# Kernel optimization log

Hardware: AMD Instinct MI355X
Metric: run time of the kernel (lower is better)

Reference implementation:

```python
import jax, jax.numpy as jnp
import numpy as np

B, N, C, K, OUT = 8, 16384, 64, 16, 64
BN_EPS = 1e-5


def setup_inputs() -> dict:
    key = jax.random.key(0)
    k1, k2, k3 = jax.random.split(key, 3)
    x = jax.random.normal(k1, (B, N, C), dtype=jnp.float32)
    idx = jax.random.randint(k2, (B, N, K), 0, N, dtype=jnp.int64)
    # fc weight, stored as (in, out) so y = agg @ W (torch Linear is x @ W.T)
    W = jax.random.normal(k3, (C, OUT), dtype=jnp.float32) * (1.0 / np.sqrt(C))
    gamma = jnp.ones((OUT,), dtype=jnp.float32)
    beta = jnp.zeros((OUT,), dtype=jnp.float32)
    return {"x": x, "idx": idx, "W": W, "gamma": gamma, "beta": beta}


def reference(x, idx, W, gamma, beta):
    Bq, Nq, Cq = x.shape
    Kq = idx.shape[-1]
    # gather neighbor features: (B, N*K, C)
    nbr = jnp.take_along_axis(x, idx.reshape(Bq, Nq * Kq, 1), axis=1)
    nbr = nbr.reshape(Bq, Nq, Kq, Cq)
    # max over neighbors, then relu
    agg = jax.nn.relu(jnp.max(nbr, axis=2))  # (B, N, C)
    # linear (no bias)
    y = agg.reshape(Bq * Nq, Cq) @ W  # (B*N, OUT)
    # BatchNorm1d in training mode: batch stats over rows, biased variance
    mean = jnp.mean(y, axis=0)
    var = jnp.mean((y - mean) ** 2, axis=0)
    y = (y - mean) * jax.lax.rsqrt(var + BN_EPS) * gamma + beta
    return y.reshape(Bq, Nq, -1)
```

## Files before the change

kernel.cpp:

```cpp
#include <hip/hip_runtime.h>

namespace {
constexpr int NPTS = 16384;
constexpr int CH   = 64;
constexpr int KNN  = 16;
constexpr int ROWS = 8 * NPTS;
constexpr float EPS = 1e-5f;
constexpr int NBLK = 1024;
constexpr int NBUCK = 16;
}

typedef __attribute__((ext_vector_type(8))) short  short8;
typedef __attribute__((ext_vector_type(4))) float  f32x4;
typedef __attribute__((ext_vector_type(4))) unsigned uint4v;
typedef __attribute__((ext_vector_type(2))) unsigned uint2v;
typedef __attribute__((ext_vector_type(4))) int    int4v;

static __device__ __forceinline__ unsigned pk_bf16(float lo, float hi) {
    unsigned r;
    asm("v_cvt_pk_bf16_f32 %0, %1, %2" : "=v"(r) : "v"(lo), "v"(hi));
    return r;
}

#define PKM(D, A, B) asm volatile("v_pk_max_i16 %0, %1, %2" : "=v"(D) : "v"(A), "v"(B))

static __device__ __host__ __forceinline__ unsigned f2bf(float f) {
    unsigned u = __builtin_bit_cast(unsigned, f);
    return (u + 0x7fffu + ((u >> 16) & 1u)) >> 16;
}

static __device__ __forceinline__ void prep_wfrags(const float* __restrict__ W,
                                                   unsigned* __restrict__ wsb, int l)
{
    const int nq = l >> 4, nr = l & 15;
#pragma unroll
    for (int ct = 0; ct < 4; ++ct)
#pragma unroll
        for (int kh = 0; kh < 2; ++kh) {
            uint4v d;
#pragma unroll
            for (int dj = 0; dj < 4; ++dj) {
                const int k0 = kh * 32 + nq * 8 + dj * 2;
                unsigned lo = f2bf(W[(size_t)k0 * CH + ct * 16 + nr]);
                unsigned hi = f2bf(W[(size_t)(k0 + 1) * CH + ct * 16 + nr]);
                d[dj] = lo | (hi << 16);
            }
            ((uint4v*)wsb)[(ct * 2 + kh) * 64 + l] = d;
        }
}

__global__ __launch_bounds__(256)
void k_cvt(const float* __restrict__ x, unsigned* __restrict__ xb16,
           const float* __restrict__ W, unsigned* __restrict__ wsb,
           float* __restrict__ stats16)
{
    if (blockIdx.x == 0) {
        if (threadIdx.x < 64) prep_wfrags(W, wsb, threadIdx.x);
        for (int i = threadIdx.x; i < NBUCK * 128; i += 256) stats16[i] = 0.f;
    }
    const int batch = blockIdx.x & 7;
    const int chunk = blockIdx.x >> 3;
    const int lane8 = threadIdx.x & 7;
    const int rr    = threadIdx.x >> 3;
    const float*  xb = x    + (size_t)batch * NPTS * CH;
    unsigned*     ob = xb16 + (size_t)batch * NPTS * 32;
#pragma unroll
    for (int h = 0; h < 2; ++h) {
        const int row = chunk * 64 + h * 32 + rr;
        const f32x4* src = (const f32x4*)(xb + (size_t)row * CH + lane8 * 8);
        f32x4 v0 = src[0], v1 = src[1];
        uint4v d;
        d[0] = pk_bf16(v0[0], v0[1]);
        d[1] = pk_bf16(v0[2], v0[3]);
        d[2] = pk_bf16(v1[0], v1[1]);
        d[3] = pk_bf16(v1[2], v1[3]);
        *(uint4v*)(ob + (size_t)row * 32 + lane8 * 4) = d;
    }
}

__global__ __launch_bounds__(256)
void k_fused_bf16(const unsigned* __restrict__ xb16, const int* __restrict__ idx,
                  const unsigned* __restrict__ wsb, unsigned* __restrict__ yp,
                  float* __restrict__ stats16)
{
    __shared__ __align__(16) ushort   Atile[4][16 * 64];
    __shared__ __align__(16) int      Ibuf[4][256];
    __shared__ __align__(16) unsigned Blds[2048];
    __shared__ float bs1[64], bs2[64];

    const int lane  = threadIdx.x & 63;
    const int wave  = threadIdx.x >> 6;
    const int batch = blockIdx.x & 7;
    const int chunk = blockIdx.x >> 3;

    ((uint4v*)Blds)[threadIdx.x]       = ((const uint4v*)wsb)[threadIdx.x];
    ((uint4v*)Blds)[threadIdx.x + 256] = ((const uint4v*)wsb)[threadIdx.x + 256];
    if (threadIdx.x < 64)       bs1[threadIdx.x] = 0.f;
    else if (threadIdx.x < 128) bs2[threadIdx.x - 64] = 0.f;
    __syncthreads();

    const unsigned* __restrict__ xb = xb16 + (size_t)batch * NPTS * 32;
    const int*      __restrict__ ib = idx  + (size_t)batch * NPTS * KNN;
    unsigned*       __restrict__ yb = yp   + (size_t)batch * NPTS * 32;

    const int r0 = chunk * 128 + wave * 16;
    const int g8 = lane >> 3, c8 = lane & 7;
    const int c4 = lane & 15, qq = lane >> 4;
    const unsigned off16 = (unsigned)c8 * 16u;
    const int key = (c4 & 7) << 4;
    char* aw = (char*)&Atile[wave][0];

    short8 bfr[8];
#pragma unroll
    for (int f = 0; f < 8; ++f)
        bfr[f] = __builtin_bit_cast(short8, ((const uint4v*)Blds)[f * 64 + lane]);

    float sC1[4] = {0.f, 0.f, 0.f, 0.f};
    float sC2[4] = {0.f, 0.f, 0.f, 0.f};

    int4v iq0 = ((const int4v*)(ib + (size_t)r0 * KNN))[lane];
    *(int4v*)&Ibuf[wave][lane * 4] = iq0;
    const int4v* Ip = (const int4v*)&Ibuf[wave][0];
    int ia[16], ibx[16];
    *(int4v*)&ia[0]  = Ip[g8 * 4 + 0];       *(int4v*)&ia[4]  = Ip[g8 * 4 + 1];
    *(int4v*)&ia[8]  = Ip[g8 * 4 + 2];       *(int4v*)&ia[12] = Ip[g8 * 4 + 3];
    *(int4v*)&ibx[0] = Ip[(g8 + 8) * 4 + 0]; *(int4v*)&ibx[4] = Ip[(g8 + 8) * 4 + 1];
    *(int4v*)&ibx[8] = Ip[(g8 + 8) * 4 + 2]; *(int4v*)&ibx[12]= Ip[(g8 + 8) * 4 + 3];

    uint4v va[16], vb[16];
#pragma unroll
    for (int j = 0; j < 16; ++j)
        asm volatile("global_load_dwordx4 %0, %1, %2"
                     : "=v"(va[j]) : "v"((unsigned)ia[j] * 128u + off16), "s"(xb));
#pragma unroll
    for (int j = 0; j < 16; ++j)
        asm volatile("global_load_dwordx4 %0, %1, %2"
                     : "=v"(vb[j]) : "v"((unsigned)ibx[j] * 128u + off16), "s"(xb));

    int4v iq1 = ((const int4v*)(ib + (size_t)(r0 + 64) * KNN))[lane];

    asm volatile("s_waitcnt vmcnt(0)" ::: "memory");
    __builtin_amdgcn_sched_barrier(0);

    uint4v accA = {0, 0, 0, 0}, accB = {0, 0, 0, 0};
#pragma unroll
    for (int j = 0; j < 16; ++j) {
        PKM(accA[0], accA[0], va[j][0]); PKM(accA[1], accA[1], va[j][1]);
        PKM(accA[2], accA[2], va[j][2]); PKM(accA[3], accA[3], va[j][3]);
    }
#pragma unroll
    for (int j = 0; j < 16; ++j) {
        PKM(accB[0], accB[0], vb[j][0]); PKM(accB[1], accB[1], vb[j][1]);
        PKM(accB[2], accB[2], vb[j][2]); PKM(accB[3], accB[3], vb[j][3]);
    }

    *(int4v*)&Ibuf[wave][lane * 4] = iq1;
    *(int4v*)&ia[0]  = Ip[g8 * 4 + 0];       *(int4v*)&ia[4]  = Ip[g8 * 4 + 1];
    *(int4v*)&ia[8]  = Ip[g8 * 4 + 2];       *(int4v*)&ia[12] = Ip[g8 * 4 + 3];
    *(int4v*)&ibx[0] = Ip[(g8 + 8) * 4 + 0]; *(int4v*)&ibx[4] = Ip[(g8 + 8) * 4 + 1];
    *(int4v*)&ibx[8] = Ip[(g8 + 8) * 4 + 2]; *(int4v*)&ibx[12]= Ip[(g8 + 8) * 4 + 3];

#pragma unroll
    for (int j = 0; j < 16; ++j)
        asm volatile("global_load_dwordx4 %0, %1, %2"
                     : "=v"(va[j]) : "v"((unsigned)ia[j] * 128u + off16), "s"(xb));
#pragma unroll
    for (int j = 0; j < 16; ++j)
        asm volatile("global_load_dwordx4 %0, %1, %2"
                     : "=v"(vb[j]) : "v"((unsigned)ibx[j] * 128u + off16), "s"(xb));
    __builtin_amdgcn_sched_barrier(0);

#define TILE_TAIL(RBASE)                                                            \
    {                                                                               \
        *(uint4v*)(aw + ((g8 * 128 + c8 * 16) ^ (g8 << 4)))       = accA;           \
        *(uint4v*)(aw + (((g8 + 8) * 128 + c8 * 16) ^ (g8 << 4))) = accB;           \
        short8 a0 = *(const short8*)(aw + ((c4 * 128 + qq * 16) ^ key));            \
        short8 a1 = *(const short8*)(aw + ((c4 * 128 + 64 + qq * 16) ^ key));       \
        f32x4 acc0 = {0,0,0,0}, acc1 = {0,0,0,0}, acc2 = {0,0,0,0}, acc3 = {0,0,0,0}; \
        acc0 = __builtin_amdgcn_mfma_f32_16x16x32_bf16(a0, bfr[0], acc0, 0, 0, 0);  \
        acc0 = __builtin_amdgcn_mfma_f32_16x16x32_bf16(a1, bfr[1], acc0, 0, 0, 0);  \
        acc1 = __builtin_amdgcn_mfma_f32_16x16x32_bf16(a0, bfr[2], acc1, 0, 0, 0);  \
        acc1 = __builtin_amdgcn_mfma_f32_16x16x32_bf16(a1, bfr[3], acc1, 0, 0, 0);  \
        acc2 = __builtin_amdgcn_mfma_f32_16x16x32_bf16(a0, bfr[4], acc2, 0, 0, 0);  \
        acc2 = __builtin_amdgcn_mfma_f32_16x16x32_bf16(a1, bfr[5], acc2, 0, 0, 0);  \
        acc3 = __builtin_amdgcn_mfma_f32_16x16x32_bf16(a0, bfr[6], acc3, 0, 0, 0);  \
        acc3 = __builtin_amdgcn_mfma_f32_16x16x32_bf16(a1, bfr[7], acc3, 0, 0, 0);  \
        unsigned* ypr = yb + (size_t)((RBASE) + qq * 4) * 32 + c4 * 2;              \
        { uint2v pr; pr[0] = pk_bf16(acc0[0], acc1[0]);                             \
          pr[1] = pk_bf16(acc2[0], acc3[0]); *(uint2v*)(ypr + 0)  = pr; }           \
        { uint2v pr; pr[0] = pk_bf16(acc0[1], acc1[1]);                             \
          pr[1] = pk_bf16(acc2[1], acc3[1]); *(uint2v*)(ypr + 32) = pr; }           \
        { uint2v pr; pr[0] = pk_bf16(acc0[2], acc1[2]);                             \
          pr[1] = pk_bf16(acc2[2], acc3[2]); *(uint2v*)(ypr + 64) = pr; }           \
        { uint2v pr; pr[0] = pk_bf16(acc0[3], acc1[3]);                             \
          pr[1] = pk_bf16(acc2[3], acc3[3]); *(uint2v*)(ypr + 96) = pr; }           \
        sC1[0] += (acc0[0] + acc0[1]) + (acc0[2] + acc0[3]);                        \
        sC2[0] += (acc0[0]*acc0[0] + acc0[1]*acc0[1]) + (acc0[2]*acc0[2] + acc0[3]*acc0[3]); \
        sC1[1] += (acc1[0] + acc1[1]) + (acc1[2] + acc1[3]);                        \
        sC2[1] += (acc1[0]*acc1[0] + acc1[1]*acc1[1]) + (acc1[2]*acc1[2] + acc1[3]*acc1[3]); \
        sC1[2] += (acc2[0] + acc2[1]) + (acc2[2] + acc2[3]);                        \
        sC2[2] += (acc2[0]*acc2[0] + acc2[1]*acc2[1]) + (acc2[2]*acc2[2] + acc2[3]*acc2[3]); \
        sC1[3] += (acc3[0] + acc3[1]) + (acc3[2] + acc3[3]);                        \
        sC2[3] += (acc3[0]*acc3[0] + acc3[1]*acc3[1]) + (acc3[2]*acc3[2] + acc3[3]*acc3[3]); \
    }

    TILE_TAIL(r0)

    asm volatile("s_waitcnt vmcnt(4)" ::: "memory");
    __builtin_amdgcn_sched_barrier(0);

    accA[0] = accA[1] = accA[2] = accA[3] = 0u;
    accB[0] = accB[1] = accB[2] = accB[3] = 0u;
#pragma unroll
    for (int j = 0; j < 16; ++j) {
        PKM(accA[0], accA[0], va[j][0]); PKM(accA[1], accA[1], va[j][1]);
        PKM(accA[2], accA[2], va[j][2]); PKM(accA[3], accA[3], va[j][3]);
    }
#pragma unroll
    for (int j = 0; j < 16; ++j) {
        PKM(accB[0], accB[0], vb[j][0]); PKM(accB[1], accB[1], vb[j][1]);
        PKM(accB[2], accB[2], vb[j][2]); PKM(accB[3], accB[3], vb[j][3]);
    }

    TILE_TAIL(r0 + 64)
#undef TILE_TAIL

#pragma unroll
    for (int ct = 0; ct < 4; ++ct) {
        float s1 = sC1[ct], s2 = sC2[ct];
        s1 += __shfl_xor(s1, 16); s1 += __shfl_xor(s1, 32);
        s2 += __shfl_xor(s2, 16); s2 += __shfl_xor(s2, 32);
        if (lane < 16) {
            atomicAdd(&bs1[ct * 16 + lane], s1);
            atomicAdd(&bs2[ct * 16 + lane], s2);
        }
    }
    __syncthreads();
    if (threadIdx.x < 128)
        atomicAdd(&stats16[(blockIdx.x & (NBUCK - 1)) * 128 + threadIdx.x],
                  (threadIdx.x < 64) ? bs1[threadIdx.x] : bs2[threadIdx.x - 64]);
}

__global__ __launch_bounds__(256)
void k_norm_bf16(const unsigned* __restrict__ yp, float* __restrict__ y,
                 const float* __restrict__ stats16,
                 const float* __restrict__ gamma, const float* __restrict__ beta)
{
    __shared__ float s[CH], b[CH];
    if (threadIdx.x < CH) {
        const int l = threadIdx.x;
        float s1 = 0.f, s2 = 0.f;
#pragma unroll
        for (int k = 0; k < NBUCK; ++k) {
            s1 += stats16[k * 128 + l];
            s2 += stats16[k * 128 + 64 + l];
        }
        const float inv_n = 1.0f / (float)ROWS;
        float mean = s1 * inv_n;
        float var  = s2 * inv_n - mean * mean;
        float sc   = gamma[l] * rsqrtf(var + EPS);
        s[l] = sc;
        b[l] = beta[l] - mean * sc;
    }
    __syncthreads();

    const size_t ntot = (size_t)ROWS * 16;
    size_t i = (size_t)blockIdx.x * blockDim.x + threadIdx.x;
    const size_t stride = (size_t)gridDim.x * blockDim.x;
    for (; i < ntot; i += stride) {
        const size_t row = i >> 4;
        const int c4 = (int)i & 15;
        uint2v p = *(const uint2v*)(yp + row * 32 + c4 * 2);
        float v0 = __uint_as_float(p[0] << 16);
        float v1 = __uint_as_float(p[0] & 0xffff0000u);
        float v2 = __uint_as_float(p[1] << 16);
        float v3 = __uint_as_float(p[1] & 0xffff0000u);
        float* yr = y + row * CH;
        yr[c4]      = fmaf(v0, s[c4],      b[c4]);
        yr[c4 + 16] = fmaf(v1, s[c4 + 16], b[c4 + 16]);
        yr[c4 + 32] = fmaf(v2, s[c4 + 32], b[c4 + 32]);
        yr[c4 + 48] = fmaf(v3, s[c4 + 48], b[c4 + 48]);
    }
}

__global__ __launch_bounds__(64)
void k_prep_fb(const float* __restrict__ W, unsigned* __restrict__ wsb,
               float* __restrict__ stats)
{
    if (threadIdx.x < 64) {
        stats[threadIdx.x] = 0.f;
        stats[64 + threadIdx.x] = 0.f;
        prep_wfrags(W, wsb, threadIdx.x);
    }
}

__global__ __launch_bounds__(256)
void k_fused_f32(const float* __restrict__ x, const int* __restrict__ idx,
                 const unsigned* __restrict__ wsb, float* __restrict__ y,
                 float* __restrict__ stats)
{
    __shared__ __align__(16) ushort Atile[4][16 * 64];
    __shared__ __align__(16) int    Ibuf[4][256];
    __shared__ float bs1[64], bs2[64];

    const int lane  = threadIdx.x & 63;
    const int wave  = threadIdx.x >> 6;
    const int batch = blockIdx.x & 7;
    const int chunk = blockIdx.x >> 3;

    if (threadIdx.x < 64)       bs1[threadIdx.x] = 0.f;
    else if (threadIdx.x < 128) bs2[threadIdx.x - 64] = 0.f;
    __syncthreads();

    const int r0 = chunk * 64 + wave * 16;
    const float* __restrict__ xb = x   + (size_t)batch * NPTS * CH;
    const int*   __restrict__ ib = idx + (size_t)batch * NPTS * KNN;
    float*       __restrict__ yb = y   + (size_t)batch * NPTS * CH;

    const int c4 = lane & 15;
    const int qq = lane >> 4;

    int4v iq = ((const int4v*)(ib + (size_t)r0 * KNN))[lane];
    *(int4v*)&Ibuf[wave][lane * 4] = iq;

    short8 bfr[8];
#pragma unroll
    for (int f = 0; f < 8; ++f)
        bfr[f] = __builtin_bit_cast(short8, ((const uint4v*)wsb)[f * 64 + lane]);

    char* aw = (char*)&Atile[wave][0];
    const f32x4* xb4 = (const f32x4*)xb;

#pragma unroll
    for (int g = 0; g < 4; ++g) {
        const int row = 4 * g + qq;
        const int* ip = &Ibuf[wave][row * KNN];
        f32x4 acc = {0.f, 0.f, 0.f, 0.f};
#pragma unroll
        for (int j = 0; j < KNN; ++j) {
            const int n = ip[j];
            f32x4 v = xb4[n * 16 + c4];
            acc[0] = fmaxf(acc[0], v[0]);
            acc[1] = fmaxf(acc[1], v[1]);
            acc[2] = fmaxf(acc[2], v[2]);
            acc[3] = fmaxf(acc[3], v[3]);
        }
        uint2v pw;
        pw[0] = pk_bf16(acc[0], acc[1]);
        pw[1] = pk_bf16(acc[2], acc[3]);
        const int wb = ((row * 128) + c4 * 8) ^ ((row & 7) << 4);
        *(uint2v*)(aw + wb) = pw;
    }

    const int key = (c4 & 7) << 4;
    short8 a0 = *(const short8*)(aw + ((c4 * 128 + qq * 16) ^ key));
    short8 a1 = *(const short8*)(aw + ((c4 * 128 + 64 + qq * 16) ^ key));

    f32x4 acc0 = {0,0,0,0}, acc1 = {0,0,0,0}, acc2 = {0,0,0,0}, acc3 = {0,0,0,0};
    acc0 = __builtin_amdgcn_mfma_f32_16x16x32_bf16(a0, bfr[0], acc0, 0, 0, 0);
    acc0 = __builtin_amdgcn_mfma_f32_16x16x32_bf16(a1, bfr[1], acc0, 0, 0, 0);
    acc1 = __builtin_amdgcn_mfma_f32_16x16x32_bf16(a0, bfr[2], acc1, 0, 0, 0);
    acc1 = __builtin_amdgcn_mfma_f32_16x16x32_bf16(a1, bfr[3], acc1, 0, 0, 0);
    acc2 = __builtin_amdgcn_mfma_f32_16x16x32_bf16(a0, bfr[4], acc2, 0, 0, 0);
    acc2 = __builtin_amdgcn_mfma_f32_16x16x32_bf16(a1, bfr[5], acc2, 0, 0, 0);
    acc3 = __builtin_amdgcn_mfma_f32_16x16x32_bf16(a0, bfr[6], acc3, 0, 0, 0);
    acc3 = __builtin_amdgcn_mfma_f32_16x16x32_bf16(a1, bfr[7], acc3, 0, 0, 0);

    float* yrow = yb + (size_t)(r0 + qq * 4) * CH + c4;
#define DO_CT(CT, ACC)                                                              \
    {                                                                               \
        yrow[0 * CH + CT * 16] = ACC[0];                                            \
        yrow[1 * CH + CT * 16] = ACC[1];                                            \
        yrow[2 * CH + CT * 16] = ACC[2];                                            \
        yrow[3 * CH + CT * 16] = ACC[3];                                            \
        float s1 = (ACC[0] + ACC[1]) + (ACC[2] + ACC[3]);                           \
        float s2 = (ACC[0]*ACC[0] + ACC[1]*ACC[1]) + (ACC[2]*ACC[2] + ACC[3]*ACC[3]); \
        s1 += __shfl_xor(s1, 16); s1 += __shfl_xor(s1, 32);                         \
        s2 += __shfl_xor(s2, 16); s2 += __shfl_xor(s2, 32);                         \
        if (lane < 16) {                                                            \
            atomicAdd(&bs1[CT * 16 + lane], s1);                                    \
            atomicAdd(&bs2[CT * 16 + lane], s2);                                    \
        }                                                                           \
    }
    DO_CT(0, acc0) DO_CT(1, acc1) DO_CT(2, acc2) DO_CT(3, acc3)
#undef DO_CT

    __syncthreads();
    if (threadIdx.x < 64)        atomicAdd(&stats[threadIdx.x], bs1[threadIdx.x]);
    else if (threadIdx.x < 128)  atomicAdd(&stats[threadIdx.x], bs2[threadIdx.x - 64]);
}

__global__ __launch_bounds__(256)
void k_norm_f32(float* __restrict__ y, const float* __restrict__ stats,
                const float* __restrict__ gamma, const float* __restrict__ beta)
{
    __shared__ float s[CH], b[CH];
    if (threadIdx.x < CH) {
        const int l = threadIdx.x;
        const float inv_n = 1.0f / (float)ROWS;
        float mean = stats[l] * inv_n;
        float var  = stats[64 + l] * inv_n - mean * mean;
        float sc   = gamma[l] * rsqrtf(var + EPS);
        s[l] = sc;
        b[l] = beta[l] - mean * sc;
    }
    __syncthreads();

    f32x4* p = (f32x4*)y;
    const size_t ntot = (size_t)ROWS * CH / 4;
    size_t i = (size_t)blockIdx.x * blockDim.x + threadIdx.x;
    const size_t stride = (size_t)gridDim.x * blockDim.x;
    for (; i < ntot; i += stride) {
        f32x4 v = p[i];
        const int c0 = ((int)i & 15) * 4;
        v[0] = fmaf(v[0], s[c0],     b[c0]);
        v[1] = fmaf(v[1], s[c0 + 1], b[c0 + 1]);
        v[2] = fmaf(v[2], s[c0 + 2], b[c0 + 2]);
        v[3] = fmaf(v[3], s[c0 + 3], b[c0 + 3]);
        p[i] = v;
    }
}

extern "C" void kernel_launch(void* const* d_in, const int* in_sizes, int n_in,
                              void* d_out, int out_size, void* d_ws, size_t ws_size,
                              hipStream_t stream)
{
    const float* x     = (const float*)d_in[0];
    const int*   idx   = (const int*)d_in[1];
    const float* W     = (const float*)d_in[2];
    const float* gamma = (const float*)d_in[3];
    const float* beta  = (const float*)d_in[4];

    float*    y       = (float*)d_out;
    float*    stats   = (float*)d_ws;
    unsigned* wsb     = (unsigned*)(stats + 256);
    char*     base    = (char*)d_ws + 16384;
    unsigned* xb16    = (unsigned*)base;
    float*    stats16 = (float*)(base + (size_t)ROWS * CH * 2);
    unsigned* yp      = (unsigned*)(stats16 + NBUCK * 128);

    const size_t need = 16384 + (size_t)ROWS * CH * 2
                      + (size_t)NBUCK * 128 * 4 + (size_t)ROWS * CH * 2;

    if (ws_size >= need) {
        k_cvt<<<dim3(2048), dim3(256), 0, stream>>>(x, xb16, W, wsb, stats16);
        k_fused_bf16<<<dim3(NBLK), dim3(256), 0, stream>>>(xb16, idx, wsb, yp, stats16);
        k_norm_bf16<<<dim3(2048), dim3(256), 0, stream>>>(yp, y, stats16, gamma, beta);
    } else {
        k_prep_fb<<<dim3(1), dim3(64), 0, stream>>>(W, wsb, stats);
        k_fused_f32<<<dim3(2048), dim3(256), 0, stream>>>(x, idx, wsb, y, stats);
        k_norm_f32<<<dim3(2048), dim3(256), 0, stream>>>(y, stats, gamma, beta);
    }
}
```

Baseline: 41.22 us.

## Process four row-tiles per block with deeper software-pipelined gather loads

Halves the block count and has each wave handle four 64-row tiles instead of two. The gather loads for the next tile, and the index load for the tile after it, are issued before the current tile's MFMA and store tail runs, using fine-grained vmcnt waits. The aim is to hide gather latency and amortise per-block setup: the weight-fragment LDS load and the stats atomics. The cost is fewer blocks in flight, which may reduce occupancy-based latency hiding, and a vmcnt accounting that must match the store counts exactly.

```diff
diff --git a/kernel.cpp b/kernel.cpp
--- a/kernel.cpp
+++ b/kernel.cpp
@@ -6,7 +6,7 @@
 constexpr int KNN  = 16;
 constexpr int ROWS = 8 * NPTS;
 constexpr float EPS = 1e-5f;
-constexpr int NBLK = 1024;
+constexpr int NBLK = 512;
 constexpr int NBUCK = 16;
 }
 
@@ -27,6 +27,29 @@
 static __device__ __host__ __forceinline__ unsigned f2bf(float f) {
     unsigned u = __builtin_bit_cast(unsigned, f);
     return (u + 0x7fffu + ((u >> 16) & 1u)) >> 16;
+}
+
+#define DRAIN(N)                                                  \
+    asm volatile("s_waitcnt vmcnt(" #N ")" ::: "memory");         \
+    __builtin_amdgcn_sched_barrier(0)
+
+static __device__ __forceinline__ void issue16(uint4v* v, const int* ix,
+                                               unsigned off16,
+                                               const unsigned* __restrict__ xb)
+{
+#pragma unroll
+    for (int j = 0; j < 16; ++j)
+        asm volatile("global_load_dwordx4 %0, %1, %2"
+                     : "=v"(v[j]) : "v"((unsigned)ix[j] * 128u + off16), "s"(xb));
+}
+
+static __device__ __forceinline__ void red16(uint4v& acc, const uint4v* v)
+{
+#pragma unroll
+    for (int j = 0; j < 16; ++j) {
+        PKM(acc[0], acc[0], v[j][0]); PKM(acc[1], acc[1], v[j][1]);
+        PKM(acc[2], acc[2], v[j][2]); PKM(acc[3], acc[3], v[j][3]);
+    }
 }
 
 static __device__ __forceinline__ void prep_wfrags(const float* __restrict__ W,
@@ -103,7 +126,7 @@
     const int*      __restrict__ ib = idx  + (size_t)batch * NPTS * KNN;
     unsigned*       __restrict__ yb = yp   + (size_t)batch * NPTS * 32;
 
-    const int r0 = chunk * 128 + wave * 16;
+    const int r0 = chunk * 256 + wave * 16;
     const int g8 = lane >> 3, c8 = lane & 7;
     const int c4 = lane & 15, qq = lane >> 4;
     const unsigned off16 = (unsigned)c8 * 16u;
@@ -118,57 +141,24 @@
     float sC1[4] = {0.f, 0.f, 0.f, 0.f};
     float sC2[4] = {0.f, 0.f, 0.f, 0.f};
 
-    int4v iq0 = ((const int4v*)(ib + (size_t)r0 * KNN))[lane];
-    *(int4v*)&Ibuf[wave][lane * 4] = iq0;
     const int4v* Ip = (const int4v*)&Ibuf[wave][0];
     int ia[16], ibx[16];
-    *(int4v*)&ia[0]  = Ip[g8 * 4 + 0];       *(int4v*)&ia[4]  = Ip[g8 * 4 + 1];
-    *(int4v*)&ia[8]  = Ip[g8 * 4 + 2];       *(int4v*)&ia[12] = Ip[g8 * 4 + 3];
-    *(int4v*)&ibx[0] = Ip[(g8 + 8) * 4 + 0]; *(int4v*)&ibx[4] = Ip[(g8 + 8) * 4 + 1];
-    *(int4v*)&ibx[8] = Ip[(g8 + 8) * 4 + 2]; *(int4v*)&ibx[12]= Ip[(g8 + 8) * 4 + 3];
-
     uint4v va[16], vb[16];
-#pragma unroll
-    for (int j = 0; j < 16; ++j)
-        asm volatile("global_load_dwordx4 %0, %1, %2"
-                     : "=v"(va[j]) : "v"((unsigned)ia[j] * 128u + off16), "s"(xb));
-#pragma unroll
-    for (int j = 0; j < 16; ++j)
-        asm volatile("global_load_dwordx4 %0, %1, %2"
-                     : "=v"(vb[j]) : "v"((unsigned)ibx[j] * 128u + off16), "s"(xb));
-
-    int4v iq1 = ((const int4v*)(ib + (size_t)(r0 + 64) * KNN))[lane];
-
-    asm volatile("s_waitcnt vmcnt(0)" ::: "memory");
-    __builtin_amdgcn_sched_barrier(0);
-
-    uint4v accA = {0, 0, 0, 0}, accB = {0, 0, 0, 0};
-#pragma unroll
-    for (int j = 0; j < 16; ++j) {
-        PKM(accA[0], accA[0], va[j][0]); PKM(accA[1], accA[1], va[j][1]);
-        PKM(accA[2], accA[2], va[j][2]); PKM(accA[3], accA[3], va[j][3]);
-    }
-#pragma unroll
-    for (int j = 0; j < 16; ++j) {
-        PKM(accB[0], accB[0], vb[j][0]); PKM(accB[1], accB[1], vb[j][1]);
-        PKM(accB[2], accB[2], vb[j][2]); PKM(accB[3], accB[3], vb[j][3]);
-    }
-
-    *(int4v*)&Ibuf[wave][lane * 4] = iq1;
-    *(int4v*)&ia[0]  = Ip[g8 * 4 + 0];       *(int4v*)&ia[4]  = Ip[g8 * 4 + 1];
-    *(int4v*)&ia[8]  = Ip[g8 * 4 + 2];       *(int4v*)&ia[12] = Ip[g8 * 4 + 3];
-    *(int4v*)&ibx[0] = Ip[(g8 + 8) * 4 + 0]; *(int4v*)&ibx[4] = Ip[(g8 + 8) * 4 + 1];
-    *(int4v*)&ibx[8] = Ip[(g8 + 8) * 4 + 2]; *(int4v*)&ibx[12]= Ip[(g8 + 8) * 4 + 3];
-
-#pragma unroll
-    for (int j = 0; j < 16; ++j)
-        asm volatile("global_load_dwordx4 %0, %1, %2"
-                     : "=v"(va[j]) : "v"((unsigned)ia[j] * 128u + off16), "s"(xb));
-#pragma unroll
-    for (int j = 0; j < 16; ++j)
-        asm volatile("global_load_dwordx4 %0, %1, %2"
-                     : "=v"(vb[j]) : "v"((unsigned)ibx[j] * 128u + off16), "s"(xb));
-    __builtin_amdgcn_sched_barrier(0);
+    uint4v accA, accB;
+    const unsigned iqoff = (unsigned)lane * 16u;
+
+#define STAGE_FROM(IQ)                                                              \
+    {                                                                               \
+        *(int4v*)&Ibuf[wave][lane * 4] = IQ;                                        \
+        *(int4v*)&ia[0]  = Ip[g8 * 4 + 0];       *(int4v*)&ia[4]  = Ip[g8 * 4 + 1]; \
+        *(int4v*)&ia[8]  = Ip[g8 * 4 + 2];       *(int4v*)&ia[12] = Ip[g8 * 4 + 3]; \
+        *(int4v*)&ibx[0] = Ip[(g8 + 8) * 4 + 0]; *(int4v*)&ibx[4] = Ip[(g8 + 8) * 4 + 1]; \
+        *(int4v*)&ibx[8] = Ip[(g8 + 8) * 4 + 2]; *(int4v*)&ibx[12]= Ip[(g8 + 8) * 4 + 3]; \
+    }
+
+#define LOAD_IQ(DST, RB)                                                            \
+    asm volatile("global_load_dwordx4 %0, %1, %2"                                   \
+                 : "=v"(DST) : "v"((unsigned)(RB) * 64u + iqoff), "s"(ib))
 
 #define TILE_TAIL(RBASE)                                                            \
     {                                                                               \
@@ -204,26 +194,55 @@
         sC2[3] += (acc3[0]*acc3[0] + acc3[1]*acc3[1]) + (acc3[2]*acc3[2] + acc3[3]*acc3[3]); \
     }
 
+#define RESET_ACC()                                                                 \
+    accA[0] = accA[1] = accA[2] = accA[3] = 0u;                                     \
+    accB[0] = accB[1] = accB[2] = accB[3] = 0u
+
+    int4v iq0 = ((const int4v*)(ib + (size_t)r0 * KNN))[lane];
+    STAGE_FROM(iq0);
+    issue16(va, ia, off16, xb);
+    issue16(vb, ibx, off16, xb);
+    int4v iq1, iq2, iq3;
+    LOAD_IQ(iq1, r0 + 64);
+    __builtin_amdgcn_sched_barrier(0);
+
+    DRAIN(1);
+    RESET_ACC(); red16(accA, va); red16(accB, vb);
+    DRAIN(0);
+    STAGE_FROM(iq1);
+    issue16(va, ia, off16, xb);
+    issue16(vb, ibx, off16, xb);
+    LOAD_IQ(iq2, r0 + 128);
+    __builtin_amdgcn_sched_barrier(0);
     TILE_TAIL(r0)
 
-    asm volatile("s_waitcnt vmcnt(4)" ::: "memory");
+    DRAIN(5);
+    RESET_ACC(); red16(accA, va); red16(accB, vb);
+    DRAIN(4);
+    STAGE_FROM(iq2);
+    issue16(va, ia, off16, xb);
+    issue16(vb, ibx, off16, xb);
+    LOAD_IQ(iq3, r0 + 192);
     __builtin_amdgcn_sched_barrier(0);
-
-    accA[0] = accA[1] = accA[2] = accA[3] = 0u;
-    accB[0] = accB[1] = accB[2] = accB[3] = 0u;
-#pragma unroll
-    for (int j = 0; j < 16; ++j) {
-        PKM(accA[0], accA[0], va[j][0]); PKM(accA[1], accA[1], va[j][1]);
-        PKM(accA[2], accA[2], va[j][2]); PKM(accA[3], accA[3], va[j][3]);
-    }
-#pragma unroll
-    for (int j = 0; j < 16; ++j) {
-        PKM(accB[0], accB[0], vb[j][0]); PKM(accB[1], accB[1], vb[j][1]);
-        PKM(accB[2], accB[2], vb[j][2]); PKM(accB[3], accB[3], vb[j][3]);
-    }
-
     TILE_TAIL(r0 + 64)
+
+    DRAIN(5);
+    RESET_ACC(); red16(accA, va); red16(accB, vb);
+    DRAIN(4);
+    STAGE_FROM(iq3);
+    issue16(va, ia, off16, xb);
+    issue16(vb, ibx, off16, xb);
+    __builtin_amdgcn_sched_barrier(0);
+    TILE_TAIL(r0 + 128)
+
+    DRAIN(4);
+    RESET_ACC(); red16(accA, va); red16(accB, vb);
+    TILE_TAIL(r0 + 192)
+
+#undef STAGE_FROM
+#undef LOAD_IQ
 #undef TILE_TAIL
+#undef RESET_ACC
 
 #pragma unroll
     for (int ct = 0; ct < 4; ++ct) {
```

After: 39.70 us. 1.04x faster.
